# Kernel optimization log

Measured on AMD Instinct MI355X. Metric: run time of the kernel, lower is better.

## Reference

```python
import jax, jax.numpy as jnp
import numpy as np

DT = 0.01          # model_config['dt']
FULL_ITERS = 30    # torchdeq f_max_iter
REUSE_ITERS = 5    # solver_kwargs={'f_max_iter': 5} when reusing w0


def setup_inputs() -> dict:
    key = jax.random.key(0)
    ks = jax.random.split(key, 16)
    B, T, IN, ST, NL, OUT, H = 2048, 32, 16, 16, 128, 8, 64
    n = lambda k, shp, s: s * jax.random.normal(k, shp, dtype=jnp.float32)
    return {
        "obs": n(ks[0], (B, T, IN), 1.0),
        "x0": jnp.zeros((B, ST), jnp.float32),
        "A_T": n(ks[1], (ST, ST), 0.25),
        "Bw_T": n(ks[2], (NL, ST), 0.08),
        "By_T": n(ks[3], (ST, ST), 0.25),
        "Cv_T": n(ks[4], (ST, NL), 0.2),
        "Dvw_T": n(ks[5], (NL, NL), 0.04),  # contractive so fixed-point iter converges
        "Dvy_T": n(ks[6], (ST, NL), 0.2),
        "Cu_T": n(ks[7], (ST, OUT), 0.25),
        "Duw_T": n(ks[8], (NL, OUT), 0.08),
        "Duy_T": n(ks[9], (ST, OUT), 0.25),
        "log_stds": jnp.full((OUT,), -1.6094379124341003, jnp.float32),
        "W1": n(ks[10], (IN, H), 1.0 / np.sqrt(IN)),
        "b1": jnp.zeros((H,), jnp.float32),
        "W2": n(ks[11], (H, H), 1.0 / np.sqrt(H)),
        "b2": jnp.zeros((H,), jnp.float32),
        "W3": n(ks[12], (H, 1), 1.0 / np.sqrt(H)),
        "b3": jnp.zeros((1,), jnp.float32),
    }


def reference(obs, x0, A_T, Bw_T, By_T, Cv_T, Dvw_T, Dvy_T, Cu_T, Duw_T,
              Duy_T, log_stds, W1, b1, W2, b2, W3, b3):
    B, T, IN = obs.shape
    NL = Dvw_T.shape[0]

    def fpi(f, w0, n_iter):
        # torchdeq fixed_point_iter: w <- f(w), n_iter times, return last iterate
        w, _ = jax.lax.scan(lambda w, _: (f(w), None), w0, None, length=n_iter)
        return w

    def xdot(x, y, w0, n_iter):
        f = lambda w: jnp.tanh(x @ Cv_T + w @ Dvw_T + y @ Dvy_T)
        w = fpi(f, w0, n_iter)
        return x @ A_T + w @ Bw_T + y @ By_T, w

    def step(x, y):
        # RK4 with y held constant over the step; w solution reused as warm start
        w_init = jnp.zeros((B, NL), x.dtype)
        k1, w1 = xdot(x, y, w_init, FULL_ITERS)
        k2, w2 = xdot(x + DT * k1 / 2, y, w1, REUSE_ITERS)
        k3, w3 = xdot(x + DT * k2 / 2, y, w2, REUSE_ITERS)
        k4, w4 = xdot(x + DT * k3, y, w3, REUSE_ITERS)
        next_x = x + DT / 6 * (k1 + 2 * k2 + 2 * k3 + k4)
        u = x @ Cu_T + w1 @ Duw_T + y @ Duy_T  # controller output at current state
        return next_x, u

    ys = jnp.swapaxes(obs, 0, 1)  # [T, B, IN]
    _, us = jax.lax.scan(step, x0, ys)  # us: [T, B, OUT]
    means = jnp.swapaxes(us, 0, 1)  # [B, T, OUT]
    log_std_b = jnp.broadcast_to(log_stds, means.shape)

    # value baseline MLP on observations
    h = jnp.tanh(obs @ W1 + b1)
    h = jnp.tanh(h @ W2 + b2)
    value = h @ W3 + b3  # [B, T, 1]

    return jnp.concatenate([means, log_std_b, value], axis=-1)  # [B, T, 2*OUT+1]
```

## Files before the change

### kernel.cpp

```cpp
#include <hip/hip_runtime.h>


typedef _Float16 f16x8 __attribute__((ext_vector_type(8)));
typedef float f32x4 __attribute__((ext_vector_type(4)));
typedef int i32x2 __attribute__((ext_vector_type(2)));
typedef int i32x4 __attribute__((ext_vector_type(4)));

constexpr int B_TOT   = 2048;
constexpr int T_STEPS = 32;
constexpr int IN_D    = 16;
constexpr int ST_D    = 16;
constexpr int NL_D    = 128;
constexpr int OUT_D   = 8;
constexpr int H_D     = 64;
constexpr int OUT_C   = 17;
constexpr float DT_F  = 0.01f;
constexpr float SC    = 2.8853900817779268f;

__device__ __forceinline__ int eperm(int s, int g, int j) {
    return 32 * s + 16 * (j >> 2) + 4 * g + (j & 3);
}

#define MFMA16(A, B, C) __builtin_amdgcn_mfma_f32_16x16x32_f16((A), (B), (C), 0, 0, 0)
#define PK(a, b) __builtin_bit_cast(int, __builtin_amdgcn_cvt_pkrtz((a), (b)))

__global__ __launch_bounds__(512, 1) void rinn_fpi(
    const float* __restrict__ obs, const float* __restrict__ x0,
    const float* __restrict__ A_T, const float* __restrict__ Bw_T,
    const float* __restrict__ By_T, const float* __restrict__ Cv_T,
    const float* __restrict__ Dvw_T, const float* __restrict__ Dvy_T,
    const float* __restrict__ Cu_T, const float* __restrict__ Duw_T,
    const float* __restrict__ Duy_T, float* __restrict__ out)
{
    __shared__ __align__(16) char xch[2][4][1024];
    const int tid  = threadIdx.x;
    const int wid  = tid >> 6;
    const int lane = tid & 63;
    const int g    = lane >> 4;
    const int r16  = lane & 15;
    const int row  = blockIdx.x * 16 + r16;
    const f32x4 z4 = {0.f, 0.f, 0.f, 0.f};

    const int c0 = wid >> 1;
    const int s1 = (c0 + 1) & 3, s2 = (c0 + 2) & 3, s3 = (c0 + 3) & 3;
    const bool hiHalf = (wid & 1);

    f16x8 aD[4];
#pragma unroll
    for (int i = 0; i < 4; ++i) {
        const int s = (c0 + i) & 3;
        f16x8 h;
#pragma unroll
        for (int j = 0; j < 8; ++j)
            h[j] = (_Float16)(SC * Dvw_T[eperm(s, g, j) * NL_D + 16 * wid + r16]);
        aD[i] = h;
    }
    f16x8 aB;
    {
        const int m = 16 * wid + r16;
        f16x8 h;
#pragma unroll
        for (int j = 0; j < 8; ++j) {
            float v = (j < 4) ? Cv_T[(4 * g + j) * NL_D + m]
                              : Dvy_T[(4 * g + (j & 3)) * NL_D + m];
            h[j] = (_Float16)(SC * v);
        }
        aB = h;
    }
    f16x8 aK[5];
    {
        f16x8 h;
#pragma unroll
        for (int j = 0; j < 8; ++j)
            h[j] = (_Float16)((j < 4) ? A_T[(4 * g + j) * ST_D + r16]
                                      : By_T[(4 * g + (j & 3)) * ST_D + r16]);
        aK[0] = h;
#pragma unroll
        for (int i = 0; i < 4; ++i) {
            const int s = (c0 + i) & 3;
            f16x8 h2;
#pragma unroll
            for (int j = 0; j < 8; ++j)
                h2[j] = (_Float16)Bw_T[eperm(s, g, j) * ST_D + r16];
            aK[1 + i] = h2;
        }
    }
    f16x8 aU[5];
    if (wid == 1) {
        f16x8 h;
#pragma unroll
        for (int j = 0; j < 8; ++j) {
            float v = 0.f;
            if (r16 < OUT_D)
                v = (j < 4) ? Cu_T[(4 * g + j) * OUT_D + r16]
                            : Duy_T[(4 * g + (j & 3)) * OUT_D + r16];
            h[j] = (_Float16)v;
        }
        aU[0] = h;
#pragma unroll
        for (int i = 0; i < 4; ++i) {
            const int s = (c0 + i) & 3;
            f16x8 h2;
#pragma unroll
            for (int j = 0; j < 8; ++j)
                h2[j] = (_Float16)((r16 < OUT_D) ? Duw_T[eperm(s, g, j) * OUT_D + r16] : 0.f);
            aU[1 + i] = h2;
        }
    } else {
#pragma unroll
        for (int s = 0; s < 5; ++s) aU[s] = __builtin_bit_cast(f16x8, z4);
    }

    f32x4 xb = *(const f32x4*)(x0 + row * ST_D + 4 * g);

    f16x8 f0, f1, f2, f3;
    int cur = 0;
    char* const xbase = &xch[0][0][0];
    const int loff = lane * 16;
    const int woff = c0 * 1024 + loff + (hiHalf ? 8 : 0);
    const int poff = c0 * 1024 + loff + (hiHalf ? 0 : 8);

    auto tanh4 = [&](f32x4 t) -> f32x4 {
        f32x4 o;
#pragma unroll
        for (int q = 0; q < 4; ++q)
            o[q] = fmaf(-2.0f, __builtin_amdgcn_rcpf(1.0f + __builtin_amdgcn_exp2f(t[q])), 1.0f);
        return o;
    };

    auto fpi = [&](int niter, f32x4 bias) {
#pragma unroll 1
        for (int it = 0; it < niter; ++it) {
            f32x4 ca = MFMA16(aD[0], f0, bias);
            f32x4 cb = MFMA16(aD[2], f2, z4);
            ca = MFMA16(aD[1], f1, ca);
            cb = MFMA16(aD[3], f3, cb);
            f32x4 v = tanh4(ca + cb);
            i32x2 own;
            own[0] = PK(v[0], v[1]);
            own[1] = PK(v[2], v[3]);
            char* nb = xbase + (cur ^ 1) * 4096;
            *(i32x2*)(nb + woff) = own;
            __syncthreads();
            i32x2 pt = *(const i32x2*)(nb + poff);
            f2 = *(const f16x8*)(nb + s2 * 1024 + loff);
            f1 = *(const f16x8*)(nb + s1 * 1024 + loff);
            f3 = *(const f16x8*)(nb + s3 * 1024 + loff);
            i32x4 oc;
            if (hiHalf) { oc[0] = pt[0]; oc[1] = pt[1]; oc[2] = own[0]; oc[3] = own[1]; }
            else        { oc[0] = own[0]; oc[1] = own[1]; oc[2] = pt[0]; oc[3] = pt[1]; }
            f0 = __builtin_bit_cast(f16x8, oc);
            cur ^= 1;
        }
    };

#pragma unroll 1
    for (int t = 0; t < T_STEPS; ++t) {
        f32x4 yb = *(const f32x4*)(obs + (row * T_STEPS + t) * IN_D + 4 * g);
        const int yw2 = PK(yb[0], yb[1]);
        const int yw3 = PK(yb[2], yb[3]);
        f0 = f1 = f2 = f3 = __builtin_bit_cast(f16x8, z4);
        f32x4 k1 = z4, k2 = z4, k3 = z4, k4 = z4;
        f32x4 xc = xb;

#pragma unroll
        for (int st = 0; st < 4; ++st) {
            int bxyw[4];
            bxyw[0] = PK(xc[0], xc[1]);
            bxyw[1] = PK(xc[2], xc[3]);
            bxyw[2] = yw2;
            bxyw[3] = yw3;
            f16x8 bXY;
            memcpy(&bXY, bxyw, 16);
            f32x4 bias = MFMA16(aB, bXY, z4);
            fpi(st ? 5 : 30, bias);
            f32x4 e0 = MFMA16(aK[0], bXY, z4);
            e0 = MFMA16(aK[1], f0, e0);
            e0 = MFMA16(aK[2], f1, e0);
            f32x4 e1 = MFMA16(aK[3], f2, z4);
            e1 = MFMA16(aK[4], f3, e1);
            f32x4 kc = e0 + e1;
            if (st == 0) {
                if (wid == 1) {
                    f32x4 u0 = MFMA16(aU[0], bXY, z4);
                    u0 = MFMA16(aU[1], f0, u0);
                    u0 = MFMA16(aU[2], f1, u0);
                    f32x4 u1 = MFMA16(aU[3], f2, z4);
                    u1 = MFMA16(aU[4], f3, u1);
                    f32x4 uc = u0 + u1;
                    if (g < 2) {
                        float* op = out + (row * T_STEPS + t) * OUT_C + 4 * g;
                        op[0] = uc[0]; op[1] = uc[1]; op[2] = uc[2]; op[3] = uc[3];
                    }
                }
                k1 = kc;
#pragma unroll
                for (int q = 0; q < 4; ++q) xc[q] = fmaf(0.5f * DT_F, k1[q], xb[q]);
            } else if (st == 1) {
                k2 = kc;
#pragma unroll
                for (int q = 0; q < 4; ++q) xc[q] = fmaf(0.5f * DT_F, k2[q], xb[q]);
            } else if (st == 2) {
                k3 = kc;
#pragma unroll
                for (int q = 0; q < 4; ++q) xc[q] = fmaf(DT_F, k3[q], xb[q]);
            } else {
                k4 = kc;
#pragma unroll
                for (int q = 0; q < 4; ++q)
                    xb[q] = fmaf(DT_F / 6.0f,
                                 k1[q] + 2.0f * k2[q] + 2.0f * k3[q] + k4[q], xb[q]);
            }
        }
    }
}

__device__ __forceinline__ float fast_tanh(float a) {
    float e = __expf(2.0f * a);
    return 1.0f - 2.0f / (e + 1.0f);
}

__global__ __launch_bounds__(256) void mlp_kernel(
    const float* __restrict__ obs, const float* __restrict__ log_stds,
    const float* __restrict__ W1, const float* __restrict__ b1,
    const float* __restrict__ W2, const float* __restrict__ b2,
    const float* __restrict__ W3, const float* __restrict__ b3,
    float* __restrict__ out) {
    __shared__ float sW1[IN_D * H_D];
    __shared__ float sW2[H_D * H_D];
    __shared__ float sb1[H_D], sb2[H_D], sW3[H_D], sls[OUT_D];
    __shared__ float sb3;
    const int tid = threadIdx.x;
    for (int i = tid; i < IN_D * H_D; i += 256) sW1[i] = W1[i];
    for (int i = tid; i < H_D * H_D; i += 256) sW2[i] = W2[i];
    if (tid < H_D) { sb1[tid] = b1[tid]; sb2[tid] = b2[tid]; sW3[tid] = W3[tid]; }
    if (tid < OUT_D) sls[tid] = log_stds[tid];
    if (tid == 0) sb3 = b3[0];
    __syncthreads();

    const int bt = blockIdx.x * 256 + tid;
    if (bt >= B_TOT * T_STEPS) return;

    float o[IN_D];
#pragma unroll
    for (int i = 0; i < IN_D; ++i) o[i] = obs[bt * IN_D + i];

    float h1[H_D];
#pragma unroll
    for (int h = 0; h < H_D; ++h) {
        float a = sb1[h];
#pragma unroll
        for (int i = 0; i < IN_D; ++i) a = fmaf(o[i], sW1[i * H_D + h], a);
        h1[h] = fast_tanh(a);
    }
    float v = sb3;
#pragma unroll
    for (int h = 0; h < H_D; ++h) {
        float a = sb2[h];
#pragma unroll
        for (int i = 0; i < H_D; ++i) a = fmaf(h1[i], sW2[i * H_D + h], a);
        v = fmaf(fast_tanh(a), sW3[h], v);
    }

    float* o17 = out + bt * OUT_C;
#pragma unroll
    for (int q = 0; q < OUT_D; ++q) o17[OUT_D + q] = sls[q];
    o17[16] = v;
}

extern "C" void kernel_launch(void* const* d_in, const int* in_sizes, int n_in,
                              void* d_out, int out_size, void* d_ws, size_t ws_size,
                              hipStream_t stream) {
    const float* obs      = (const float*)d_in[0];
    const float* x0       = (const float*)d_in[1];
    const float* A_T      = (const float*)d_in[2];
    const float* Bw_T     = (const float*)d_in[3];
    const float* By_T     = (const float*)d_in[4];
    const float* Cv_T     = (const float*)d_in[5];
    const float* Dvw_T    = (const float*)d_in[6];
    const float* Dvy_T    = (const float*)d_in[7];
    const float* Cu_T     = (const float*)d_in[8];
    const float* Duw_T    = (const float*)d_in[9];
    const float* Duy_T    = (const float*)d_in[10];
    const float* log_stds = (const float*)d_in[11];
    const float* W1       = (const float*)d_in[12];
    const float* b1       = (const float*)d_in[13];
    const float* W2       = (const float*)d_in[14];
    const float* b2       = (const float*)d_in[15];
    const float* W3       = (const float*)d_in[16];
    const float* b3       = (const float*)d_in[17];
    float* out = (float*)d_out;

    rinn_fpi<<<dim3(B_TOT / 16), dim3(512), 0, stream>>>(
        obs, x0, A_T, Bw_T, By_T, Cv_T, Dvw_T, Dvy_T, Cu_T, Duw_T, Duy_T, out);
    mlp_kernel<<<dim3((B_TOT * T_STEPS + 255) / 256), dim3(256), 0, stream>>>(
        obs, log_stds, W1, b1, W2, b2, W3, b3, out);
}
```

Measured before the change: 452.0 us.

## Shrink FPI block to two waves, each computing four NL tiles

Each block of the recurrent fixed-point kernel drops from eight waves to two. Each wave now owns 64 of the 128 nonlinearity outputs and issues 16 MFMAs per iteration, spread over four independent accumulator chains. The goal is a cheaper per-iteration __syncthreads and less LDS exchange, since a wave's own half of w is reused straight from registers. In exchange each wave does four times the MFMA and tanh work per iteration, holds many more weight fragments in registers, and the grid keeps only 128 small blocks.

```diff
diff --git a/kernel.cpp b/kernel.cpp
--- a/kernel.cpp
+++ b/kernel.cpp
@@ -3,7 +3,6 @@
 
 typedef _Float16 f16x8 __attribute__((ext_vector_type(8)));
 typedef float f32x4 __attribute__((ext_vector_type(4)));
-typedef int i32x2 __attribute__((ext_vector_type(2)));
 typedef int i32x4 __attribute__((ext_vector_type(4)));
 
 constexpr int B_TOT   = 2048;
@@ -24,7 +23,7 @@
 #define MFMA16(A, B, C) __builtin_amdgcn_mfma_f32_16x16x32_f16((A), (B), (C), 0, 0, 0)
 #define PK(a, b) __builtin_bit_cast(int, __builtin_amdgcn_cvt_pkrtz((a), (b)))
 
-__global__ __launch_bounds__(512, 1) void rinn_fpi(
+__global__ __launch_bounds__(128, 1) void rinn_fpi(
     const float* __restrict__ obs, const float* __restrict__ x0,
     const float* __restrict__ A_T, const float* __restrict__ Bw_T,
     const float* __restrict__ By_T, const float* __restrict__ Cv_T,
@@ -41,23 +40,27 @@
     const int row  = blockIdx.x * 16 + r16;
     const f32x4 z4 = {0.f, 0.f, 0.f, 0.f};
 
-    const int c0 = wid >> 1;
-    const int s1 = (c0 + 1) & 3, s2 = (c0 + 2) & 3, s3 = (c0 + 3) & 3;
-    const bool hiHalf = (wid & 1);
-
-    f16x8 aD[4];
-#pragma unroll
-    for (int i = 0; i < 4; ++i) {
-        const int s = (c0 + i) & 3;
-        f16x8 h;
-#pragma unroll
-        for (int j = 0; j < 8; ++j)
-            h[j] = (_Float16)(SC * Dvw_T[eperm(s, g, j) * NL_D + 16 * wid + r16]);
-        aD[i] = h;
-    }
-    f16x8 aB;
-    {
-        const int m = 16 * wid + r16;
+    const int co0 = 2 * wid,           co1 = 2 * wid + 1;
+    const int cf0 = (2 * wid + 2) & 3, cf1 = (2 * wid + 3) & 3;
+
+    f16x8 aD[4][4];
+#pragma unroll
+    for (int t4 = 0; t4 < 4; ++t4) {
+        const int m = 16 * (4 * wid + t4) + r16;
+#pragma unroll
+        for (int i = 0; i < 4; ++i) {
+            const int s = (2 * wid + i) & 3;
+            f16x8 h;
+#pragma unroll
+            for (int j = 0; j < 8; ++j)
+                h[j] = (_Float16)(SC * Dvw_T[eperm(s, g, j) * NL_D + m]);
+            aD[t4][i] = h;
+        }
+    }
+    f16x8 aB[4];
+#pragma unroll
+    for (int t4 = 0; t4 < 4; ++t4) {
+        const int m = 16 * (4 * wid + t4) + r16;
         f16x8 h;
 #pragma unroll
         for (int j = 0; j < 8; ++j) {
@@ -65,7 +68,7 @@
                               : Dvy_T[(4 * g + (j & 3)) * NL_D + m];
             h[j] = (_Float16)(SC * v);
         }
-        aB = h;
+        aB[t4] = h;
     }
     f16x8 aK[5];
     {
@@ -77,7 +80,7 @@
         aK[0] = h;
 #pragma unroll
         for (int i = 0; i < 4; ++i) {
-            const int s = (c0 + i) & 3;
+            const int s = (2 * wid + i) & 3;
             f16x8 h2;
 #pragma unroll
             for (int j = 0; j < 8; ++j)
@@ -99,7 +102,7 @@
         aU[0] = h;
 #pragma unroll
         for (int i = 0; i < 4; ++i) {
-            const int s = (c0 + i) & 3;
+            const int s = (2 * wid + i) & 3;
             f16x8 h2;
 #pragma unroll
             for (int j = 0; j < 8; ++j)
@@ -117,8 +120,6 @@
     int cur = 0;
     char* const xbase = &xch[0][0][0];
     const int loff = lane * 16;
-    const int woff = c0 * 1024 + loff + (hiHalf ? 8 : 0);
-    const int poff = c0 * 1024 + loff + (hiHalf ? 0 : 8);
 
     auto tanh4 = [&](f32x4 t) -> f32x4 {
         f32x4 o;
@@ -128,28 +129,48 @@
         return o;
     };
 
-    auto fpi = [&](int niter, f32x4 bias) {
+    f32x4 bA0, bA1, bA2, bA3;
+
+    auto fpi = [&](int niter) {
 #pragma unroll 1
         for (int it = 0; it < niter; ++it) {
-            f32x4 ca = MFMA16(aD[0], f0, bias);
-            f32x4 cb = MFMA16(aD[2], f2, z4);
-            ca = MFMA16(aD[1], f1, ca);
-            cb = MFMA16(aD[3], f3, cb);
-            f32x4 v = tanh4(ca + cb);
-            i32x2 own;
-            own[0] = PK(v[0], v[1]);
-            own[1] = PK(v[2], v[3]);
+            f32x4 a0 = MFMA16(aD[0][0], f0, bA0);
+            f32x4 a1 = MFMA16(aD[1][0], f0, bA1);
+            f32x4 a2 = MFMA16(aD[2][0], f0, bA2);
+            f32x4 a3 = MFMA16(aD[3][0], f0, bA3);
+            a0 = MFMA16(aD[0][1], f1, a0);
+            a1 = MFMA16(aD[1][1], f1, a1);
+            a2 = MFMA16(aD[2][1], f1, a2);
+            a3 = MFMA16(aD[3][1], f1, a3);
+            f32x4 b0 = MFMA16(aD[0][2], f2, z4);
+            f32x4 b1 = MFMA16(aD[1][2], f2, z4);
+            f32x4 b2 = MFMA16(aD[2][2], f2, z4);
+            f32x4 b3 = MFMA16(aD[3][2], f2, z4);
+            b0 = MFMA16(aD[0][3], f3, b0);
+            b1 = MFMA16(aD[1][3], f3, b1);
+            b2 = MFMA16(aD[2][3], f3, b2);
+            b3 = MFMA16(aD[3][3], f3, b3);
+            f32x4 v0 = tanh4(a0 + b0);
+            f32x4 v1 = tanh4(a1 + b1);
+            f32x4 v2 = tanh4(a2 + b2);
+            f32x4 v3 = tanh4(a3 + b3);
+            i32x4 own0, own1;
+            own0[0] = PK(v0[0], v0[1]);
+            own0[1] = PK(v0[2], v0[3]);
+            own0[2] = PK(v1[0], v1[1]);
+            own0[3] = PK(v1[2], v1[3]);
+            own1[0] = PK(v2[0], v2[1]);
+            own1[1] = PK(v2[2], v2[3]);
+            own1[2] = PK(v3[0], v3[1]);
+            own1[3] = PK(v3[2], v3[3]);
             char* nb = xbase + (cur ^ 1) * 4096;
-            *(i32x2*)(nb + woff) = own;
+            *(i32x4*)(nb + co0 * 1024 + loff) = own0;
+            *(i32x4*)(nb + co1 * 1024 + loff) = own1;
             __syncthreads();
-            i32x2 pt = *(const i32x2*)(nb + poff);
-            f2 = *(const f16x8*)(nb + s2 * 1024 + loff);
-            f1 = *(const f16x8*)(nb + s1 * 1024 + loff);
-            f3 = *(const f16x8*)(nb + s3 * 1024 + loff);
-            i32x4 oc;
-            if (hiHalf) { oc[0] = pt[0]; oc[1] = pt[1]; oc[2] = own[0]; oc[3] = own[1]; }
-            else        { oc[0] = own[0]; oc[1] = own[1]; oc[2] = pt[0]; oc[3] = pt[1]; }
-            f0 = __builtin_bit_cast(f16x8, oc);
+            f0 = __builtin_bit_cast(f16x8, own0);
+            f1 = __builtin_bit_cast(f16x8, own1);
+            f2 = *(const f16x8*)(nb + cf0 * 1024 + loff);
+            f3 = *(const f16x8*)(nb + cf1 * 1024 + loff);
             cur ^= 1;
         }
     };
@@ -172,8 +193,11 @@
             bxyw[3] = yw3;
             f16x8 bXY;
             memcpy(&bXY, bxyw, 16);
-            f32x4 bias = MFMA16(aB, bXY, z4);
-            fpi(st ? 5 : 30, bias);
+            bA0 = MFMA16(aB[0], bXY, z4);
+            bA1 = MFMA16(aB[1], bXY, z4);
+            bA2 = MFMA16(aB[2], bXY, z4);
+            bA3 = MFMA16(aB[3], bXY, z4);
+            fpi(st ? 5 : 30);
             f32x4 e0 = MFMA16(aK[0], bXY, z4);
             e0 = MFMA16(aK[1], f0, e0);
             e0 = MFMA16(aK[2], f1, e0);
@@ -291,7 +315,7 @@
     const float* b3       = (const float*)d_in[17];
     float* out = (float*)d_out;
 
-    rinn_fpi<<<dim3(B_TOT / 16), dim3(512), 0, stream>>>(
+    rinn_fpi<<<dim3(B_TOT / 16), dim3(128), 0, stream>>>(
         obs, x0, A_T, Bw_T, By_T, Cv_T, Dvw_T, Dvy_T, Cu_T, Duw_T, Duy_T, out);
     mlp_kernel<<<dim3((B_TOT * T_STEPS + 255) / 256), dim3(256), 0, stream>>>(
         obs, log_stds, W1, b1, W2, b2, W3, b3, out);
```

After: 681.5 us. +50.8%, slower.
